# Optimization experiments

Measured on AMD Instinct MI355X. Metric: run time of the kernel, lower is better.

The kernel has to match this reference:

```python
import jax, jax.numpy as jnp
import numpy as np

ALPHA = 0.2   # LeakyReLU slope
V = 7         # graph nodes (hard-coded 7x7 adjacency in source)
BN_EPS = 1e-5


def _leaky(x):
    return jnp.where(x >= 0, x, ALPHA * x)


def _norm_adj(B):
    # adj = min-max normalized (B + I), then D^{-1/2} adj D^{-1/2}
    adj = B + jnp.eye(V, dtype=B.dtype)
    adj = (adj - adj.min()) / (adj.max() - adj.min())
    inv = 1.0 / jnp.sqrt(jnp.sum(adj, axis=1))
    return adj * inv[:, None] * inv[None, :]


def _gat1_head(h_flat, W, a, B):
    # h_flat: (N, V, C*T)=  (N,7,180); W: (180,9); a: (18,1); B: (7,7)
    Wh = h_flat @ W                       # (N, V, E)
    E = W.shape[1]
    s_i = Wh @ a[:E, 0]                   # (N, V)  == [Wh_i ; .] part of concat score
    s_j = Wh @ a[E:, 0]                   # (N, V)  == [. ; Wh_j] part
    e = _leaky(s_i[:, :, None] + s_j[:, None, :])   # (N, V, V)
    att = jax.nn.softmax(e, axis=-1)
    adjn = _norm_adj(B)
    att = jnp.einsum('ik,nkj->nij', adjn, att)      # adj_norm @ attention
    return jax.nn.elu(att @ Wh)           # (N, V, E)


def _gat2_head(h, W, a, B):
    # h: (N, V, C, 30); W: (30,10); a: (20,1); B: (7,7)
    Wh = h @ W                            # (N, V, C, F)
    F = W.shape[1]
    s_i = jnp.einsum('nvcf,f->nvc', Wh, a[:F, 0])
    s_j = jnp.einsum('nvcf,f->nvc', Wh, a[F:, 0])
    e = _leaky(s_i[:, :, None, :] + s_j[:, None, :, :])   # (N, V, V, C)
    att = jax.nn.softmax(e, axis=-1)      # softmax over channel dim (as in source)
    # nested V-loop with diag_embed == weighted sum over j, per-channel scaling
    h2 = jnp.einsum('njcf,nijc->ncfi', Wh, att)           # (N, C, F, V)
    adjn = _norm_adj(B)
    out = jnp.einsum('ncfu,uv->ncfv', h2, adjn)
    return jax.nn.elu(out)                # (N, C, F, V)


def setup_inputs() -> dict:
    key = jax.random.key(0)
    ks = jax.random.split(key, 16)
    N, C, T = 32768, 6, 30
    f32 = jnp.float32
    inp = {
        'x': jax.random.normal(ks[0], (N, C, T, V), f32),
        'bn_gamma': jax.random.uniform(ks[1], (42,), f32, 0.5, 1.5),
        'bn_beta': 0.1 * jax.random.normal(ks[2], (42,), f32),
        'W1': 0.1 * jax.random.normal(ks[3], (20, 180, 9), f32),
        'a1': 0.1 * jax.random.normal(ks[4], (20, 18, 1), f32),
        'B1': 0.01 * jax.random.uniform(ks[5], (20, V, V), f32) + 1e-6,
        'W2': 0.1 * jax.random.normal(ks[6], (3, 30, 10), f32),
        'a2': 0.1 * jax.random.normal(ks[7], (3, 20, 1), f32),
        'B2': 0.01 * jax.random.uniform(ks[8], (3, V, V), f32) + 1e-6,
        'W_ih': 0.1 * jax.random.normal(ks[9], (84, 84), f32),
        'W_hh': 0.1 * jax.random.normal(ks[10], (84, 21), f32),
        'b_ih': 0.1 * jax.random.normal(ks[11], (84,), f32),
        'b_hh': 0.1 * jax.random.normal(ks[12], (84,), f32),
        'W_out': 0.1 * jax.random.normal(ks[13], (7, 21), f32),
        'b_out': 0.1 * jax.random.normal(ks[14], (7,), f32),
    }
    return inp


def reference(x, bn_gamma, bn_beta, W1, a1, B1, W2, a2, B2,
              W_ih, W_hh, b_ih, b_hh, W_out, b_out):
    N, C, T, _ = x.shape                  # (N, 6, 30, 7)
    # data_bn: BatchNorm1d(42) in train mode (batch stats over N and T)
    xb = jnp.transpose(x, (0, 3, 1, 2)).reshape(N, V * C, T)
    mean = jnp.mean(xb, axis=(0, 2), keepdims=True)
    var = jnp.var(xb, axis=(0, 2), keepdims=True)
    xb = (xb - mean) / jnp.sqrt(var + BN_EPS)
    xb = xb * bn_gamma[None, :, None] + bn_beta[None, :, None]
    x0 = jnp.transpose(xb.reshape(N, V, C, T), (0, 2, 3, 1))   # (N, C, T, V)

    # l1: 20-head GAT on flattened (C*T) node features
    h_flat = jnp.transpose(x0, (0, 3, 1, 2)).reshape(N, V, C * T)
    heads1 = jax.vmap(_gat1_head, in_axes=(None, 0, 0, 0))(h_flat, W1, a1, B1)  # (20,N,V,9)
    x1 = jnp.moveaxis(heads1, 0, 2).reshape(N, V, C * T)       # cat over heads, last dim
    x1 = jnp.transpose(x1.reshape(N, V, C, T), (0, 2, 3, 1))   # (N, C, T, V)

    # l2: 3-head 2D GAT over the T axis
    h2in = jnp.transpose(x0, (0, 3, 1, 2))                      # (N, V, C, T)
    heads2 = jax.vmap(_gat2_head, in_axes=(None, 0, 0, 0))(h2in, W2, a2, B2)  # (3,N,C,10,V)
    x2 = jnp.moveaxis(heads2, 0, 2).reshape(N, C, 30, V)        # cat over heads on dim=2

    xcat = jnp.concatenate([x1, x2], axis=1)                    # (N, 12, 30, 7)

    # RNN head: source takes r_out[:, 0, :], so only LSTM step 0 (h0=c0=0) matters
    xs = jnp.transpose(xcat, (0, 2, 1, 3)).reshape(N, T, 84)
    gates = xs[:, 0, :] @ W_ih.T + b_ih + b_hh                  # h0=0 => W_hh term vanishes
    i_g, f_g, g_g, o_g = jnp.split(gates, 4, axis=-1)           # torch gate order i,f,g,o
    c1 = jax.nn.sigmoid(i_g) * jnp.tanh(g_g)
    h1 = jax.nn.sigmoid(o_g) * jnp.tanh(c1)
    return h1 @ W_out.T + b_out                                 # (N, 7)
```

## Files before the change

### kernel.cpp

```cpp
#include <hip/hip_runtime.h>

#define F1260 1260

__device__ __forceinline__ float leakyf(float x) { return x >= 0.f ? x : 0.2f * x; }
__device__ __forceinline__ float eluf(float x) { return x > 0.f ? x : expm1f(x); }
__device__ __forceinline__ float sigmoidf(float x) { return 1.f / (1.f + __expf(-x)); }
__device__ __forceinline__ float tanh_fast(float x) { return 1.f - 2.f / (__expf(2.f * x) + 1.f); }


__global__ __launch_bounds__(320) void kA_stats(const float* __restrict__ x,
                                                float* __restrict__ ws, int N) {
    const int t = threadIdx.x;
    if (t >= 315) return;
    const int n0 = blockIdx.x * 128;
    const int f0 = t * 4;
    float s0 = 0.f, s1 = 0.f, s2 = 0.f, s3 = 0.f;
    float q0 = 0.f, q1 = 0.f, q2 = 0.f, q3 = 0.f;
#pragma unroll 8
    for (int i = 0; i < 128; ++i) {
        const float4 a = *(const float4*)(x + (size_t)(n0 + i) * F1260 + f0);
        s0 += a.x; q0 += a.x * a.x;
        s1 += a.y; q1 += a.y * a.y;
        s2 += a.z; q2 += a.z * a.z;
        s3 += a.w; q3 += a.w * a.w;
    }
    atomicAdd(&ws[f0 + 0], s0);
    atomicAdd(&ws[f0 + 1], s1);
    atomicAdd(&ws[f0 + 2], s2);
    atomicAdd(&ws[f0 + 3], s3);
    atomicAdd(&ws[1280 + f0 + 0], q0);
    atomicAdd(&ws[1280 + f0 + 1], q1);
    atomicAdd(&ws[1280 + f0 + 2], q2);
    atomicAdd(&ws[1280 + f0 + 3], q3);
}

__global__ __launch_bounds__(256) void kB_setup(
        const float* __restrict__ bn_gamma, const float* __restrict__ bn_beta,
        const float* __restrict__ W1, const float* __restrict__ a1, const float* __restrict__ B1,
        const float* __restrict__ W2, const float* __restrict__ a2, const float* __restrict__ B2,
        const float* __restrict__ b_ih, const float* __restrict__ b_hh,
        const float* __restrict__ W_out, const float* __restrict__ b_out,
        float* __restrict__ ws, int N) {
    const int t = threadIdx.x;
    float* pb = ws + 2560;
    const int HH[6] = {0, 3, 6, 10, 13, 16};
    const int EH[6] = {0, 3, 6, 0, 3, 6};

    if (t < 42) {
        const int v = t / 6, c = t % 6;
        float s = 0.f, q = 0.f;
        for (int tt = 0; tt < 30; ++tt) {
            const int f = c * 210 + tt * 7 + v;
            s += ws[f];
            q += ws[1280 + f];
        }
        const float cnt = 30.f * (float)N;
        const float mean = s / cnt;
        const float var = q / cnt - mean * mean;
        const float sc = bn_gamma[t] * rsqrtf(var + 1e-5f);
        pb[t] = sc;
        pb[64 + t] = bn_beta[t] - mean * sc;
    }
    if (t >= 64 && t < 71) {
        const int idx = t - 64;
        const float* Bp = (idx < 6) ? (B1 + HH[idx] * 49) : B2;
        float* op = pb + 128 + idx * 49;
        float adj[49];
        for (int i = 0; i < 49; ++i) adj[i] = Bp[i];
        for (int i = 0; i < 7; ++i) adj[i * 8] += 1.f;
        float mn = adj[0], mx = adj[0];
        for (int i = 1; i < 49; ++i) { mn = fminf(mn, adj[i]); mx = fmaxf(mx, adj[i]); }
        const float inv = 1.f / (mx - mn);
        float rinv[7];
        for (int i = 0; i < 7; ++i) {
            float rs = 0.f;
            for (int j = 0; j < 7; ++j) { adj[i * 7 + j] = (adj[i * 7 + j] - mn) * inv; rs += adj[i * 7 + j]; }
            rinv[i] = rsqrtf(rs);
        }
        for (int i = 0; i < 7; ++i)
            for (int j = 0; j < 7; ++j)
                op[i * 7 + j] = adj[i * 7 + j] * rinv[i] * rinv[j];
    }
    for (int task = t; task < 6 * 180; task += 256) {
        const int hh = task / 180, k = task % 180;
        const int h = HH[hh];
        const float* Wp = W1 + ((size_t)h * 180 + k) * 9;
        float si = 0.f, sj = 0.f;
        for (int e = 0; e < 9; ++e) {
            const float w = Wp[e];
            si += w * a1[h * 18 + e];
            sj += w * a1[h * 18 + 9 + e];
        }
        pb[512 + k * 24 + hh * 3 + 0] = si;
        pb[512 + k * 24 + hh * 3 + 1] = sj;
        pb[512 + k * 24 + hh * 3 + 2] = Wp[EH[hh]];
    }
    if (t < 30) {
        const float* Wp = W2 + t * 10;
        float si = 0.f, sj = 0.f;
        for (int f = 0; f < 10; ++f) {
            const float w = Wp[f];
            si += w * a2[f];
            sj += w * a2[10 + f];
        }
        for (int c = 0; c < 6; ++c) {
            const int k = c * 30 + t;
            pb[512 + k * 24 + 18] = si;
            pb[512 + k * 24 + 19] = sj;
            pb[512 + k * 24 + 20] = Wp[0];
        }
    }
    if (t < 84) pb[4832 + t] = b_ih[t] + b_hh[t];
    if (t < 147) pb[4928 + t] = W_out[t];
    if (t < 7) pb[5078 + t] = b_out[t];
}

#define RS 252
__global__ __launch_bounds__(64) void kC_main(const float* __restrict__ x,
        const float* __restrict__ pb, const float* __restrict__ Wih,
        float* __restrict__ outp, int N) {
    __shared__ __align__(16) float sm[3627];
    float* res  = sm;
    float* xs0  = sm + 2016;
    float* h2t  = sm + 2688;
    float* h1s  = sm + 3024;
    float* scsh = sm + 3200;
    float* adjL = sm + 3284;

    const int t = threadIdx.x;
    const int n0 = blockIdx.x * 8;

    for (int i = t; i < 84; i += 64) scsh[i] = pb[i < 42 ? i : 22 + i];
    for (int i = t; i < 343; i += 64) adjL[i] = pb[128 + i];
    __syncthreads();

    const int v = t >> 3, nl = t & 7;
    if (v < 7) {
        float s1[18];
#pragma unroll
        for (int i = 0; i < 18; ++i) s1[i] = 0.f;
        const float* xb = x + (size_t)(n0 + nl) * F1260 + v;
        const float* WB = pb + 512;
        for (int c = 0; c < 6; ++c) {
            const float sc = scsh[v * 6 + c];
            const float sh = scsh[42 + v * 6 + c];
            const float* xr = xb + c * 210;
            const float* wb = WB + (c * 30) * 24;
            float xv[30];
#pragma unroll
            for (int tt = 0; tt < 30; ++tt) xv[tt] = xr[tt * 7];
            float g0 = 0.f, g1 = 0.f, g2 = 0.f;
#pragma unroll
            for (int tt = 0; tt < 30; ++tt) {
                const float a = xv[tt] * sc + sh;
                const float* w = wb + tt * 24;
#pragma unroll
                for (int q = 0; q < 18; ++q) s1[q] += a * w[q];
                g0 += a * w[18];
                g1 += a * w[19];
                g2 += a * w[20];
            }
            float* rp = res + nl * RS + 126 + (v * 6 + c) * 3;
            rp[0] = g0; rp[1] = g1; rp[2] = g2;
        }
#pragma unroll
        for (int q = 0; q < 18; ++q)
            res[nl * RS + v * 18 + q] = s1[q];
    }
    __syncthreads();

    if (t < 48) {
        const int hh = t >> 3, nl2 = t & 7;
        float si[7], sj[7], we[7];
#pragma unroll
        for (int vv = 0; vv < 7; ++vv) {
            const float* rp = res + nl2 * RS + vv * 18 + hh * 3;
            si[vv] = rp[0]; sj[vv] = rp[1]; we[vv] = rp[2];
        }
        float mxsj = sj[0];
#pragma unroll
        for (int j = 1; j < 7; ++j) mxsj = fmaxf(mxsj, sj[j]);
        float p[7];
#pragma unroll
        for (int i = 0; i < 7; ++i) {
            const float m = leakyf(si[i] + mxsj);
            float den = 0.f, num = 0.f;
#pragma unroll
            for (int j = 0; j < 7; ++j) {
                const float w = __expf(leakyf(si[i] + sj[j]) - m);
                den += w;
                num += w * we[j];
            }
            p[i] = num / den;
        }
        const float* An = adjL + hh * 49;
#pragma unroll
        for (int i = 0; i < 7; ++i) {
            float r = 0.f;
#pragma unroll
            for (int k = 0; k < 7; ++k) r += An[i * 7 + k] * p[k];
            xs0[nl2 * 84 + hh * 7 + i] = eluf(r);
        }
    }
    if (t < 56) {
        const int i = t >> 3, nl2 = t & 7;
        float si2[6];
#pragma unroll
        for (int c = 0; c < 6; ++c)
            si2[c] = res[nl2 * RS + 126 + (i * 6 + c) * 3];
        float hc[6];
#pragma unroll
        for (int c = 0; c < 6; ++c) hc[c] = 0.f;
#pragma unroll
        for (int j = 0; j < 7; ++j) {
            float s[6];
            float m = -1e30f;
#pragma unroll
            for (int c = 0; c < 6; ++c) {
                const float* rp = res + nl2 * RS + 126 + (j * 6 + c) * 3;
                s[c] = leakyf(si2[c] + rp[1]);
                m = fmaxf(m, s[c]);
            }
            float den = 0.f;
#pragma unroll
            for (int c = 0; c < 6; ++c) { s[c] = __expf(s[c] - m); den += s[c]; }
            const float rd = 1.f / den;
#pragma unroll
            for (int c = 0; c < 6; ++c) {
                const float wh0 = res[nl2 * RS + 126 + (j * 6 + c) * 3 + 2];
                hc[c] += wh0 * s[c] * rd;
            }
        }
#pragma unroll
        for (int c = 0; c < 6; ++c)
            h2t[nl2 * 42 + i * 6 + c] = hc[c];
    }
    __syncthreads();

    if (t < 48) {
        const int c = t >> 3, nl2 = t & 7;
        const float* An2 = adjL + 6 * 49;
        float h[7];
#pragma unroll
        for (int u = 0; u < 7; ++u) h[u] = h2t[nl2 * 42 + u * 6 + c];
#pragma unroll
        for (int vv = 0; vv < 7; ++vv) {
            float r = 0.f;
#pragma unroll
            for (int u = 0; u < 7; ++u) r += h[u] * An2[u * 7 + vv];
            xs0[nl2 * 84 + 42 + c * 7 + vv] = eluf(r);
        }
    }
    __syncthreads();

    {
        const int g8 = t >> 3, nl2 = t & 7;
        const float* bias = pb + 4832;
        const float4* xs4 = (const float4*)(xs0 + nl2 * 84);
        for (int gi = g8; gi < 21; gi += 8) {
            float ga = bias[gi], gg = bias[42 + gi], go = bias[63 + gi];
            const float4* wa = (const float4*)(Wih + gi * 84);
            const float4* wg = (const float4*)(Wih + (42 + gi) * 84);
            const float4* wo = (const float4*)(Wih + (63 + gi) * 84);
#pragma unroll
            for (int k = 0; k < 21; ++k) {
                const float4 xv = xs4[k];
                const float4 a4 = wa[k];
                const float4 g4 = wg[k];
                const float4 o4 = wo[k];
                ga += xv.x * a4.x + xv.y * a4.y + xv.z * a4.z + xv.w * a4.w;
                gg += xv.x * g4.x + xv.y * g4.y + xv.z * g4.z + xv.w * g4.w;
                go += xv.x * o4.x + xv.y * o4.y + xv.z * o4.z + xv.w * o4.w;
            }
            const float c1 = sigmoidf(ga) * tanh_fast(gg);
            h1s[nl2 * 22 + gi] = sigmoidf(go) * tanh_fast(c1);
        }
    }
    __syncthreads();

    if (t < 56) {
        const int nl2 = t / 7, j = t - nl2 * 7;
        const float* Wout = pb + 4928;
        float r = pb[5078 + j];
#pragma unroll
        for (int m = 0; m < 21; ++m) r += h1s[nl2 * 22 + m] * Wout[j * 21 + m];
        outp[(size_t)n0 * 7 + t] = r;
    }
}

extern "C" void kernel_launch(void* const* d_in, const int* in_sizes, int n_in,
                              void* d_out, int out_size, void* d_ws, size_t ws_size,
                              hipStream_t stream) {
    const int N = in_sizes[0] / F1260;

    const float* x        = (const float*)d_in[0];
    const float* bn_gamma = (const float*)d_in[1];
    const float* bn_beta  = (const float*)d_in[2];
    const float* W1       = (const float*)d_in[3];
    const float* a1       = (const float*)d_in[4];
    const float* B1       = (const float*)d_in[5];
    const float* W2       = (const float*)d_in[6];
    const float* a2       = (const float*)d_in[7];
    const float* B2       = (const float*)d_in[8];
    const float* W_ih     = (const float*)d_in[9];
    const float* b_ih     = (const float*)d_in[11];
    const float* b_hh     = (const float*)d_in[12];
    const float* W_out    = (const float*)d_in[13];
    const float* b_out    = (const float*)d_in[14];

    float* wsf = (float*)d_ws;

    hipMemsetAsync(d_ws, 0, 2560 * sizeof(float), stream);

    kA_stats<<<dim3(N / 128), dim3(320), 0, stream>>>(x, wsf, N);
    kB_setup<<<dim3(1), dim3(256), 0, stream>>>(bn_gamma, bn_beta, W1, a1, B1,
                                                W2, a2, B2, b_ih, b_hh,
                                                W_out, b_out, wsf, N);
    kC_main<<<dim3(N / 8), dim3(64), 0, stream>>>(x, wsf + 2560, W_ih, (float*)d_out, N);
}
```

Measured before the change: 390.5 us.

## Replace global atomics in BN stats with per-block partials and drop memset

The statistics kernel now runs a fixed 128 blocks, each covering N/128 rows. Each block reduces its sums over the T axis in shared memory and writes 84 per-channel partials to its own workspace slot, instead of issuing atomics on 2520 floats from 256 blocks. The setup kernel then sums the 128 partials, so the memset launch is no longer needed. The trade-off is fewer blocks for a read of about 165MB, which may underuse the GPU's compute units and memory bandwidth.

```diff
diff --git a/kernel.cpp b/kernel.cpp
--- a/kernel.cpp
+++ b/kernel.cpp
@@ -1,6 +1,8 @@
 #include <hip/hip_runtime.h>
 
 #define F1260 1260
+#define NPART 128
+#define PB_OFF 10752
 
 __device__ __forceinline__ float leakyf(float x) { return x >= 0.f ? x : 0.2f * x; }
 __device__ __forceinline__ float eluf(float x) { return x > 0.f ? x : expm1f(x); }
@@ -9,29 +11,40 @@
 
 
 __global__ __launch_bounds__(320) void kA_stats(const float* __restrict__ x,
-                                                float* __restrict__ ws, int N) {
+                                                float* __restrict__ ws, int rows) {
+    __shared__ float fs[1260], fq[1260];
     const int t = threadIdx.x;
-    if (t >= 315) return;
-    const int n0 = blockIdx.x * 128;
-    const int f0 = t * 4;
-    float s0 = 0.f, s1 = 0.f, s2 = 0.f, s3 = 0.f;
-    float q0 = 0.f, q1 = 0.f, q2 = 0.f, q3 = 0.f;
-#pragma unroll 8
-    for (int i = 0; i < 128; ++i) {
-        const float4 a = *(const float4*)(x + (size_t)(n0 + i) * F1260 + f0);
-        s0 += a.x; q0 += a.x * a.x;
-        s1 += a.y; q1 += a.y * a.y;
-        s2 += a.z; q2 += a.z * a.z;
-        s3 += a.w; q3 += a.w * a.w;
-    }
-    atomicAdd(&ws[f0 + 0], s0);
-    atomicAdd(&ws[f0 + 1], s1);
-    atomicAdd(&ws[f0 + 2], s2);
-    atomicAdd(&ws[f0 + 3], s3);
-    atomicAdd(&ws[1280 + f0 + 0], q0);
-    atomicAdd(&ws[1280 + f0 + 1], q1);
-    atomicAdd(&ws[1280 + f0 + 2], q2);
-    atomicAdd(&ws[1280 + f0 + 3], q3);
+    const int n0 = blockIdx.x * rows;
+    if (t < 315) {
+        const int f0 = t * 4;
+        float s0 = 0.f, s1 = 0.f, s2 = 0.f, s3 = 0.f;
+        float q0 = 0.f, q1 = 0.f, q2 = 0.f, q3 = 0.f;
+#pragma unroll 16
+        for (int i = 0; i < rows; ++i) {
+            const float4 a = *(const float4*)(x + (size_t)(n0 + i) * F1260 + f0);
+            s0 += a.x; q0 += a.x * a.x;
+            s1 += a.y; q1 += a.y * a.y;
+            s2 += a.z; q2 += a.z * a.z;
+            s3 += a.w; q3 += a.w * a.w;
+        }
+        fs[f0 + 0] = s0; fq[f0 + 0] = q0;
+        fs[f0 + 1] = s1; fq[f0 + 1] = q1;
+        fs[f0 + 2] = s2; fq[f0 + 2] = q2;
+        fs[f0 + 3] = s3; fq[f0 + 3] = q3;
+    }
+    __syncthreads();
+    if (t < 42) {
+        const int v = t / 6, c = t % 6;
+        float s = 0.f, q = 0.f;
+#pragma unroll
+        for (int tt = 0; tt < 30; ++tt) {
+            const int f = c * 210 + tt * 7 + v;
+            s += fs[f];
+            q += fq[f];
+        }
+        ws[blockIdx.x * 84 + t] = s;
+        ws[blockIdx.x * 84 + 42 + t] = q;
+    }
 }
 
 __global__ __launch_bounds__(256) void kB_setup(
@@ -42,17 +55,15 @@
         const float* __restrict__ W_out, const float* __restrict__ b_out,
         float* __restrict__ ws, int N) {
     const int t = threadIdx.x;
-    float* pb = ws + 2560;
+    float* pb = ws + PB_OFF;
     const int HH[6] = {0, 3, 6, 10, 13, 16};
     const int EH[6] = {0, 3, 6, 0, 3, 6};
 
     if (t < 42) {
-        const int v = t / 6, c = t % 6;
         float s = 0.f, q = 0.f;
-        for (int tt = 0; tt < 30; ++tt) {
-            const int f = c * 210 + tt * 7 + v;
-            s += ws[f];
-            q += ws[1280 + f];
+        for (int b = 0; b < NPART; ++b) {
+            s += ws[b * 84 + t];
+            q += ws[b * 84 + 42 + t];
         }
         const float cnt = 30.f * (float)N;
         const float mean = s / cnt;
@@ -310,11 +321,10 @@
 
     float* wsf = (float*)d_ws;
 
-    hipMemsetAsync(d_ws, 0, 2560 * sizeof(float), stream);
-
-    kA_stats<<<dim3(N / 128), dim3(320), 0, stream>>>(x, wsf, N);
+
+    kA_stats<<<dim3(NPART), dim3(320), 0, stream>>>(x, wsf, N / NPART);
     kB_setup<<<dim3(1), dim3(256), 0, stream>>>(bn_gamma, bn_beta, W1, a1, B1,
                                                 W2, a2, B2, b_ih, b_hh,
                                                 W_out, b_out, wsf, N);
-    kC_main<<<dim3(N / 8), dim3(64), 0, stream>>>(x, wsf + 2560, W_ih, (float*)d_out, N);
+    kC_main<<<dim3(N / 8), dim3(64), 0, stream>>>(x, wsf + PB_OFF, W_ih, (float*)d_out, N);
 }
```

New measurement: 368.5 us. 1.06x faster.
